# Performance work log

Hardware: AMD Instinct MI355X
Metric: run time of the kernel (lower is better)

## Reference

```python
import jax, jax.numpy as jnp
import numpy as np

NUM_EMBEDDINGS = 8192
EMBEDDING_DIM = 128
COMMITMENT_COST = 0.02


def _l2_normalize(x, axis=-1, eps=1e-12):
    # matches torch F.normalize: x / max(||x||, eps)
    n = jnp.sqrt(jnp.sum(x * x, axis=axis, keepdims=True))
    return x / jnp.maximum(n, eps)


def setup_inputs() -> dict:
    key = jax.random.key(0)
    k1, k2 = jax.random.split(key)
    inputs = jax.random.normal(k1, (16, 128, 2048), dtype=jnp.float32)  # [B, D, T]
    lim = 1.0 / NUM_EMBEDDINGS
    codebook = jax.random.uniform(k2, (NUM_EMBEDDINGS, EMBEDDING_DIM),
                                  dtype=jnp.float32, minval=-lim, maxval=lim)
    return {"inputs": inputs, "codebook": codebook}


def reference(inputs, codebook):
    # inputs: [B, D, T] -> [B, T, D]
    x = jnp.transpose(inputs, (0, 2, 1))
    B, T, D = x.shape
    flat = x.reshape(-1, D)                      # [N, D]
    flat_n = _l2_normalize(flat, axis=1)         # [N, D]
    emb_n = _l2_normalize(codebook, axis=1)      # [K, D]
    # cosine-style distance: 2 - 2 * <x_hat, e_hat>
    distances = 2.0 - 2.0 * jnp.einsum('nd,kd->nk', flat_n, emb_n)  # [N, K]
    encoding_indices = jnp.argmin(distances, axis=1)[:, None]       # [N, 1]
    # (dead-code revival is a training-time RNG side effect on the codebook;
    #  eval path / reference math skips it)
    quantized = codebook[encoding_indices[:, 0]].reshape(B, T, D)   # [B, T, D]
    sg = jax.lax.stop_gradient
    e_latent_loss = jnp.mean((sg(quantized) - x) ** 2)
    q_latent_loss = jnp.mean((quantized - sg(x)) ** 2)
    loss = q_latent_loss + COMMITMENT_COST * e_latent_loss
    # straight-through estimator
    quantized_st = x + sg(quantized - x)
    out = jnp.transpose(quantized_st, (0, 2, 1))  # back to [B, D, T]
    return loss, out, encoding_indices
```

## Files before the change

### kernel.cpp

```cpp
#include <hip/hip_runtime.h>
#include <hip/hip_bf16.h>

#define NROWS 32768
#define KCODES 8192
#define DDIM 128
#define TT 2048
#define ETOT 4194304

typedef __attribute__((ext_vector_type(8))) _Float16 f16x8;
typedef __attribute__((ext_vector_type(4))) float f32x4;

__device__ __forceinline__ float pk(float v, int p) {
    return __int_as_float((__float_as_int(v) & 0xFFFFE000) | p);
}

__device__ __forceinline__ void async16(char* lds_uniform, const char* g_perlane) {
    __builtin_amdgcn_global_load_lds(
        (const __attribute__((address_space(1))) unsigned int*)g_perlane,
        (__attribute__((address_space(3))) unsigned int*)lds_uniform,
        16, 0, 0);
}

#define SYNC2 asm volatile("s_waitcnt vmcnt(2) lgkmcnt(0)\n\ts_barrier" ::: "memory")
#define SYNC0 asm volatile("s_waitcnt vmcnt(0) lgkmcnt(0)\n\ts_barrier" ::: "memory")

__global__ void k_en_prep(const float* __restrict__ cb,
                          _Float16* __restrict__ eh) {
    int w = (blockIdx.x * blockDim.x + threadIdx.x) >> 6;
    int l = threadIdx.x & 63;
    if (w >= KCODES) return;
    const float* row = cb + (long)w * DDIM;
    float v0 = row[l], v1 = row[l + 64];
    float ss = v0 * v0 + v1 * v1;
#pragma unroll
    for (int s = 1; s < 64; s <<= 1) ss += __shfl_xor(ss, s, 64);
    float inv = 1.0f / fmaxf(sqrtf(ss), 1e-12f);
    int tile = w >> 4, c = w & 15;
#pragma unroll
    for (int e = 0; e < 2; e++) {
        int d = l + e * 64;
        float v = (e ? v1 : v0) * inv;
        int ks = d >> 5, kq = (d >> 3) & 3, dr = d & 7;
        long off = (long)tile * 2048 + ks * 512 + (kq * 16 + c) * 8 + dr;
        eh[off] = (_Float16)v;
    }
}

__global__ void k_x_prep(const float* __restrict__ in,
                         _Float16* __restrict__ xh) {
    __shared__ float tb[64][65];
    int bid = blockIdx.x;
    int tt0 = (bid & 31) * 64;
    int dd0 = ((bid >> 5) & 1) * 64;
    int b = bid >> 6;
    const float* base = in + (long)b * DDIM * TT;
    int tl = threadIdx.x & 63;
    int dg = threadIdx.x >> 6;
#pragma unroll
    for (int i = 0; i < 16; i++) {
        int dd = dg + i * 4;
        tb[dd][tl] = base[(long)(dd0 + dd) * TT + tt0 + tl];
    }
    __syncthreads();
    int dl = threadIdx.x & 63;
    int tg = threadIdx.x >> 6;
#pragma unroll
    for (int i = 0; i < 16; i++) {
        int t = tg + i * 4;
        long n = (long)b * TT + tt0 + t;
        xh[n * DDIM + dd0 + dl] = (_Float16)tb[dl][t];
    }
}

__device__ __forceinline__ void mfma4(const char* buf, int l,
                                      const f16x8 (&bx)[4][4], f32x4 (&acc)[4]) {
    const f32x4 Z = {0.f, 0.f, 0.f, 0.f};
    f16x8 ah[4];
#pragma unroll
    for (int ks = 0; ks < 4; ks++)
        ah[ks] = *(const f16x8*)(buf + ks * 1024 + l * 16);
    __builtin_amdgcn_s_setprio(1);
#pragma unroll
    for (int nf = 0; nf < 4; nf++) {
        f32x4 a = __builtin_amdgcn_mfma_f32_16x16x32_f16(ah[0], bx[nf][0], Z, 0, 0, 0);
        a = __builtin_amdgcn_mfma_f32_16x16x32_f16(ah[1], bx[nf][1], a, 0, 0, 0);
        a = __builtin_amdgcn_mfma_f32_16x16x32_f16(ah[2], bx[nf][2], a, 0, 0, 0);
        acc[nf] = __builtin_amdgcn_mfma_f32_16x16x32_f16(ah[3], bx[nf][3], a, 0, 0, 0);
    }
    __builtin_amdgcn_s_setprio(0);
}

__device__ __forceinline__ void sel4(const f32x4 (&acc)[4], int PP,
                                     float (&t1)[4], float (&t2)[4], float (&u1)[4]) {
#pragma unroll
    for (int nf = 0; nf < 4; nf++) {
        f32x4 a = acc[nf];
        float s0 = pk(a[0], PP),     s1 = pk(a[1], PP - 1);
        float s2 = pk(a[2], PP - 2), s3 = pk(a[3], PP - 3);
        float h01 = fmaxf(s0, s1), l01 = fminf(s0, s1);
        float h23 = fmaxf(s2, s3), l23 = fminf(s2, s3);
        float m1 = fmaxf(h01, h23);
        float m2 = fmaxf(fminf(h01, h23), fmaxf(l01, l23));
        float n1 = fminf(t1[nf], m1); t1[nf] = fmaxf(t1[nf], m1);
        t2[nf] = fmaxf(t2[nf], n1);
        u1[nf] = fmaxf(u1[nf], m2);
    }
}

__global__ __launch_bounds__(256, 3) void k_main(const _Float16* __restrict__ xh,
                                                 const _Float16* __restrict__ eh,
                                                 int* __restrict__ cand) {
    extern __shared__ char lds[];
    const int tid = threadIdx.x;
    const int l = tid & 63;
    const int w = tid >> 6;
    const int e8 = blockIdx.x & 7;
    const int rb = blockIdx.x >> 3;
    const int col = l & 15, kq = l >> 4;
    const long rbase = (long)rb * 256;

    f16x8 bx[4][4];
#pragma unroll
    for (int nf = 0; nf < 4; nf++) {
        long n = rbase + w * 64 + nf * 16 + col;
#pragma unroll
        for (int ks = 0; ks < 4; ks++)
            bx[nf][ks] = *(const f16x8*)(xh + n * DDIM + ks * 32 + kq * 8);
    }

    const float NEG = __int_as_float(0xFF800000);
    float t1[4], t2[4], u1[4];
#pragma unroll
    for (int i = 0; i < 4; i++) { t1[i] = t2[i] = u1[i] = NEG; }

    int P = 8191 - (e8 * 1024 + kq * 4);

    const char* gsrc = (const char*)eh + (long)e8 * 262144 + w * 1024 + l * 16;
    char* b0 = lds;
    char* b1 = lds + 8192;
    char* b2 = lds + 16384;

    async16(b0 + w * 1024, gsrc);
    async16(b0 + 4096 + w * 1024, gsrc + 4096);
    async16(b1 + w * 1024, gsrc + 8192);
    async16(b1 + 4096 + w * 1024, gsrc + 12288);

    f32x4 accA[4], accB[4];
    int PA, PB;

    SYNC2;
    async16(b2 + w * 1024, gsrc + 2 * 8192);
    async16(b2 + 4096 + w * 1024, gsrc + 2 * 8192 + 4096);
    mfma4(b0, l, bx, accA); PA = P; P -= 16;
    mfma4(b0 + 4096, l, bx, accB); PB = P; P -= 16;
    sel4(accA, PA, t1, t2, u1);
    { char* tp = b0; b0 = b1; b1 = b2; b2 = tp; }

    for (int p = 1; p <= 30; ++p) {
        SYNC2;
        if (p < 30) {
            async16(b2 + w * 1024, gsrc + (long)(p + 2) * 8192);
            async16(b2 + 4096 + w * 1024, gsrc + (long)(p + 2) * 8192 + 4096);
        }
        mfma4(b0, l, bx, accA); PA = P; P -= 16;
        sel4(accB, PB, t1, t2, u1);
        mfma4(b0 + 4096, l, bx, accB); PB = P; P -= 16;
        sel4(accA, PA, t1, t2, u1);
        { char* tp = b0; b0 = b1; b1 = b2; b2 = tp; }
    }
    SYNC0;
    mfma4(b0, l, bx, accA); PA = P; P -= 16;
    sel4(accB, PB, t1, t2, u1);
    mfma4(b0 + 4096, l, bx, accB); PB = P;
    sel4(accA, PA, t1, t2, u1);
    sel4(accB, PB, t1, t2, u1);

    __syncthreads();
    float* mrg = (float*)lds;
#pragma unroll
    for (int nf = 0; nf < 4; nf++) {
        int row = w * 64 + nf * 16 + col;
        int e = kq * 3;
        mrg[row * 13 + e + 0] = t1[nf];
        mrg[row * 13 + e + 1] = t2[nf];
        mrg[row * 13 + e + 2] = u1[nf];
    }
    __syncthreads();
    {
        float s1 = NEG, s2 = NEG;
#pragma unroll 4
        for (int e = 0; e < 12; e++) {
            float v = mrg[tid * 13 + e];
            float a1 = fminf(s1, v); s1 = fmaxf(s1, v);
            s2 = fmaxf(s2, a1);
        }
        long n = rbase + tid;
        int* cp = cand + n * 16 + e8 * 2;
        cp[0] = 8191 - (__float_as_int(s1) & 0x1FFF);
        cp[1] = 8191 - (__float_as_int(s2) & 0x1FFF);
    }
}

__global__ void k_rf(const float* __restrict__ in, const float* __restrict__ cb,
                     const int* __restrict__ cand, float* __restrict__ out,
                     float* __restrict__ idx_f, double* __restrict__ part) {
    __shared__ float xs[16][132];
    __shared__ int sbi[16];
    __shared__ double sd[256];
    const int tid = threadIdx.x;
    const int n0 = blockIdx.x * 16;
    const int b = n0 >> 11, t0 = n0 & 2047;

    {
        int d = tid >> 1, h = tid & 1;
        const float* src = in + ((long)b * DDIM + d) * TT + t0 + h * 8;
        float4 v0 = *(const float4*)src;
        float4 v1 = *(const float4*)(src + 4);
#pragma unroll
        for (int j = 0; j < 4; j++) {
            xs[h * 8 + j][d] = ((const float*)&v0)[j];
            xs[h * 8 + 4 + j][d] = ((const float*)&v1)[j];
        }
    }
    __syncthreads();

    {
        int r = tid >> 4, k = tid & 15;
        int n = n0 + r;
        int c = cand[n * 16 + k];
        const float4* e = (const float4*)(cb + (long)c * DDIM);
        double dot = 0.0, nrm = 0.0;
        for (int d4 = 0; d4 < 32; d4++) {
            float4 q = e[d4];
#pragma unroll
            for (int j = 0; j < 4; j++) {
                double xd = (double)xs[r][d4 * 4 + j];
                double f = (double)((const float*)&q)[j];
                dot += xd * f;
                nrm += f * f;
            }
        }
        double sv = dot / fmax(sqrt(nrm), 1e-12);
#pragma unroll
        for (int s = 1; s < 16; s <<= 1) {
            double osv = __shfl_xor(sv, s, 64);
            int oc = __shfl_xor(c, s, 64);
            if (osv > sv || (osv == sv && oc < c)) { sv = osv; c = oc; }
        }
        if (k == 0) {
            sbi[r] = c;
            idx_f[n] = (float)c;
        }
    }
    __syncthreads();

    {
        int d = tid >> 1, h = tid & 1;
        float* ob = out + ((long)b * DDIM + d) * TT + t0 + h * 8;
        double acc = 0.0;
        float ov[8];
#pragma unroll
        for (int j = 0; j < 8; j++) {
            int rr = h * 8 + j;
            float xv = xs[rr][d];
            float qv = cb[(long)sbi[rr] * DDIM + d];
            float diff = qv - xv;
            ov[j] = xv + diff;
            acc += (double)diff * (double)diff;
        }
        *(float4*)ob = make_float4(ov[0], ov[1], ov[2], ov[3]);
        *(float4*)(ob + 4) = make_float4(ov[4], ov[5], ov[6], ov[7]);
        sd[tid] = acc;
    }
    __syncthreads();
    for (int s = 128; s > 0; s >>= 1) {
        if (tid < s) sd[tid] += sd[tid + s];
        __syncthreads();
    }
    if (tid == 0) part[blockIdx.x] = sd[0];
}

__global__ void k_loss_final(const double* __restrict__ part, int np,
                             float* __restrict__ loss) {
    __shared__ double sd[256];
    double a = 0.0;
    for (int i = threadIdx.x; i < np; i += 256) a += part[i];
    sd[threadIdx.x] = a;
    __syncthreads();
    for (int s = 128; s > 0; s >>= 1) {
        if (threadIdx.x < s) sd[threadIdx.x] += sd[threadIdx.x + s];
        __syncthreads();
    }
    if (threadIdx.x == 0) {
        float m = (float)(sd[0] / (double)ETOT);
        loss[0] = m + 0.02f * m;
    }
}

extern "C" void kernel_launch(void* const* d_in, const int* in_sizes, int n_in,
                              void* d_out, int out_size, void* d_ws, size_t ws_size,
                              hipStream_t stream) {
    const float* inputs = (const float*)d_in[0];
    const float* cb     = (const float*)d_in[1];
    float* outf = (float*)d_out;

    char* ws = (char*)d_ws;
    _Float16* xh = (_Float16*)ws; ws += (long)NROWS * DDIM * 2;
    _Float16* eh = (_Float16*)ws; ws += (long)KCODES * DDIM * 2;
    int* cand    = (int*)ws;      ws += (long)NROWS * 16 * 4;
    double* part = (double*)ws;   ws += 2048 * 8;

    k_en_prep<<<dim3(2048), dim3(256), 0, stream>>>(cb, eh);
    k_x_prep<<<dim3(1024), dim3(256), 0, stream>>>(inputs, xh);
    k_main<<<dim3(1024), dim3(256), 24576, stream>>>(xh, eh, cand);
    k_rf<<<dim3(2048), dim3(256), 0, stream>>>(inputs, cb, cand, outf + 1,
                                               outf + 1 + (long)ETOT, part);
    k_loss_final<<<dim3(1), dim3(256), 0, stream>>>(part, 2048, outf);
}
```

Measured before the change: 138.2 us.

## Merge prep kernels, interleave MFMA chains, unroll triple-buffer rotation with constant offsets

Merges the codebook-normalise and input-transpose prep kernels into one launch, with block index selecting the role. This removes a kernel launch and lets both prep jobs run concurrently. Reorders the MFMA sequence so the four independent accumulator chains are interleaved per k-step, which removes back-to-back dependent MFMAs. Unrolls the triple-buffered LDS pipeline by three so buffer addresses are compile-time offsets instead of rotating pointers, at the cost of more code size.

After: 285.6 us. 107% more time.

```diff
diff --git a/kernel.cpp b/kernel.cpp
--- a/kernel.cpp
+++ b/kernel.cpp
@@ -24,56 +24,56 @@
 #define SYNC2 asm volatile("s_waitcnt vmcnt(2) lgkmcnt(0)\n\ts_barrier" ::: "memory")
 #define SYNC0 asm volatile("s_waitcnt vmcnt(0) lgkmcnt(0)\n\ts_barrier" ::: "memory")
 
-__global__ void k_en_prep(const float* __restrict__ cb,
-                          _Float16* __restrict__ eh) {
-    int w = (blockIdx.x * blockDim.x + threadIdx.x) >> 6;
-    int l = threadIdx.x & 63;
-    if (w >= KCODES) return;
-    const float* row = cb + (long)w * DDIM;
-    float v0 = row[l], v1 = row[l + 64];
-    float ss = v0 * v0 + v1 * v1;
-#pragma unroll
-    for (int s = 1; s < 64; s <<= 1) ss += __shfl_xor(ss, s, 64);
-    float inv = 1.0f / fmaxf(sqrtf(ss), 1e-12f);
-    int tile = w >> 4, c = w & 15;
-#pragma unroll
-    for (int e = 0; e < 2; e++) {
-        int d = l + e * 64;
-        float v = (e ? v1 : v0) * inv;
-        int ks = d >> 5, kq = (d >> 3) & 3, dr = d & 7;
-        long off = (long)tile * 2048 + ks * 512 + (kq * 16 + c) * 8 + dr;
-        eh[off] = (_Float16)v;
-    }
-}
-
-__global__ void k_x_prep(const float* __restrict__ in,
-                         _Float16* __restrict__ xh) {
+__global__ void k_prep(const float* __restrict__ cb, _Float16* __restrict__ eh,
+                       const float* __restrict__ in, _Float16* __restrict__ xh) {
     __shared__ float tb[64][65];
     int bid = blockIdx.x;
-    int tt0 = (bid & 31) * 64;
-    int dd0 = ((bid >> 5) & 1) * 64;
-    int b = bid >> 6;
-    const float* base = in + (long)b * DDIM * TT;
-    int tl = threadIdx.x & 63;
-    int dg = threadIdx.x >> 6;
-#pragma unroll
-    for (int i = 0; i < 16; i++) {
-        int dd = dg + i * 4;
-        tb[dd][tl] = base[(long)(dd0 + dd) * TT + tt0 + tl];
-    }
-    __syncthreads();
-    int dl = threadIdx.x & 63;
-    int tg = threadIdx.x >> 6;
-#pragma unroll
-    for (int i = 0; i < 16; i++) {
-        int t = tg + i * 4;
-        long n = (long)b * TT + tt0 + t;
-        xh[n * DDIM + dd0 + dl] = (_Float16)tb[dl][t];
-    }
-}
-
-__device__ __forceinline__ void mfma4(const char* buf, int l,
-                                      const f16x8 (&bx)[4][4], f32x4 (&acc)[4]) {
+    if (bid < 2048) {
+        int w = (bid * blockDim.x + threadIdx.x) >> 6;
+        int l = threadIdx.x & 63;
+        if (w >= KCODES) return;
+        const float* row = cb + (long)w * DDIM;
+        float v0 = row[l], v1 = row[l + 64];
+        float ss = v0 * v0 + v1 * v1;
+#pragma unroll
+        for (int s = 1; s < 64; s <<= 1) ss += __shfl_xor(ss, s, 64);
+        float inv = 1.0f / fmaxf(sqrtf(ss), 1e-12f);
+        int tile = w >> 4, c = w & 15;
+#pragma unroll
+        for (int e = 0; e < 2; e++) {
+            int d = l + e * 64;
+            float v = (e ? v1 : v0) * inv;
+            int ks = d >> 5, kq = (d >> 3) & 3, dr = d & 7;
+            long off = (long)tile * 2048 + ks * 512 + (kq * 16 + c) * 8 + dr;
+            eh[off] = (_Float16)v;
+        }
+    } else {
+        bid -= 2048;
+        int tt0 = (bid & 31) * 64;
+        int dd0 = ((bid >> 5) & 1) * 64;
+        int b = bid >> 6;
+        const float* base = in + (long)b * DDIM * TT;
+        int tl = threadIdx.x & 63;
+        int dg = threadIdx.x >> 6;
+#pragma unroll
+        for (int i = 0; i < 16; i++) {
+            int dd = dg + i * 4;
+            tb[dd][tl] = base[(long)(dd0 + dd) * TT + tt0 + tl];
+        }
+        __syncthreads();
+        int dl = threadIdx.x & 63;
+        int tg = threadIdx.x >> 6;
+#pragma unroll
+        for (int i = 0; i < 16; i++) {
+            int t = tg + i * 4;
+            long n = (long)b * TT + tt0 + t;
+            xh[n * DDIM + dd0 + dl] = (_Float16)tb[dl][t];
+        }
+    }
+}
+
+__device__ __forceinline__ void mfma4i(const char* buf, int l,
+                                       const f16x8 (&bx)[4][4], f32x4 (&acc)[4]) {
     const f32x4 Z = {0.f, 0.f, 0.f, 0.f};
     f16x8 ah[4];
 #pragma unroll
@@ -81,12 +81,13 @@
         ah[ks] = *(const f16x8*)(buf + ks * 1024 + l * 16);
     __builtin_amdgcn_s_setprio(1);
 #pragma unroll
-    for (int nf = 0; nf < 4; nf++) {
-        f32x4 a = __builtin_amdgcn_mfma_f32_16x16x32_f16(ah[0], bx[nf][0], Z, 0, 0, 0);
-        a = __builtin_amdgcn_mfma_f32_16x16x32_f16(ah[1], bx[nf][1], a, 0, 0, 0);
-        a = __builtin_amdgcn_mfma_f32_16x16x32_f16(ah[2], bx[nf][2], a, 0, 0, 0);
-        acc[nf] = __builtin_amdgcn_mfma_f32_16x16x32_f16(ah[3], bx[nf][3], a, 0, 0, 0);
-    }
+    for (int nf = 0; nf < 4; nf++)
+        acc[nf] = __builtin_amdgcn_mfma_f32_16x16x32_f16(ah[0], bx[nf][0], Z, 0, 0, 0);
+#pragma unroll
+    for (int ks = 1; ks < 4; ks++)
+#pragma unroll
+        for (int nf = 0; nf < 4; nf++)
+            acc[nf] = __builtin_amdgcn_mfma_f32_16x16x32_f16(ah[ks], bx[nf][ks], acc[nf], 0, 0, 0);
     __builtin_amdgcn_s_setprio(0);
 }
 
@@ -136,42 +137,49 @@
     int P = 8191 - (e8 * 1024 + kq * 4);
 
     const char* gsrc = (const char*)eh + (long)e8 * 262144 + w * 1024 + l * 16;
-    char* b0 = lds;
-    char* b1 = lds + 8192;
-    char* b2 = lds + 16384;
-
-    async16(b0 + w * 1024, gsrc);
-    async16(b0 + 4096 + w * 1024, gsrc + 4096);
-    async16(b1 + w * 1024, gsrc + 8192);
-    async16(b1 + 4096 + w * 1024, gsrc + 12288);
+    const int wo = w * 1024;
+
+    async16(lds + wo, gsrc);
+    async16(lds + 4096 + wo, gsrc + 4096);
+    async16(lds + 8192 + wo, gsrc + 8192);
+    async16(lds + 8192 + 4096 + wo, gsrc + 12288);
 
     f32x4 accA[4], accB[4];
     int PA, PB;
 
     SYNC2;
-    async16(b2 + w * 1024, gsrc + 2 * 8192);
-    async16(b2 + 4096 + w * 1024, gsrc + 2 * 8192 + 4096);
-    mfma4(b0, l, bx, accA); PA = P; P -= 16;
-    mfma4(b0 + 4096, l, bx, accB); PB = P; P -= 16;
+    async16(lds + 16384 + wo, gsrc + 2 * 8192);
+    async16(lds + 16384 + 4096 + wo, gsrc + 2 * 8192 + 4096);
+    mfma4i(lds, l, bx, accA); PA = P; P -= 16;
+    mfma4i(lds + 4096, l, bx, accB); PB = P; P -= 16;
     sel4(accA, PA, t1, t2, u1);
-    { char* tp = b0; b0 = b1; b1 = b2; b2 = tp; }
-
-    for (int p = 1; p <= 30; ++p) {
-        SYNC2;
-        if (p < 30) {
-            async16(b2 + w * 1024, gsrc + (long)(p + 2) * 8192);
-            async16(b2 + 4096 + w * 1024, gsrc + (long)(p + 2) * 8192 + 4096);
-        }
-        mfma4(b0, l, bx, accA); PA = P; P -= 16;
-        sel4(accB, PB, t1, t2, u1);
-        mfma4(b0 + 4096, l, bx, accB); PB = P; P -= 16;
-        sel4(accA, PA, t1, t2, u1);
-        { char* tp = b0; b0 = b1; b1 = b2; b2 = tp; }
-    }
+
+#define PHASE(RD, ST, PHN)                                                     \
+    {                                                                          \
+        SYNC2;                                                                 \
+        if ((PHN) < 30) {                                                      \
+            async16(lds + (ST) + wo, gsrc + (long)((PHN) + 2) * 8192);         \
+            async16(lds + (ST) + 4096 + wo,                                    \
+                    gsrc + (long)((PHN) + 2) * 8192 + 4096);                   \
+        }                                                                      \
+        mfma4i(lds + (RD), l, bx, accA); PA = P; P -= 16;                      \
+        sel4(accB, PB, t1, t2, u1);                                            \
+        mfma4i(lds + (RD) + 4096, l, bx, accB); PB = P; P -= 16;               \
+        sel4(accA, PA, t1, t2, u1);                                            \
+    }
+
+    for (int i = 0; i < 10; ++i) {
+        int p = 3 * i;
+        PHASE(8192,  0,     p + 1);
+        PHASE(16384, 8192,  p + 2);
+        PHASE(0,     16384, p + 3);
+    }
+#undef PHASE
+
     SYNC0;
-    mfma4(b0, l, bx, accA); PA = P; P -= 16;
+    mfma4i(lds + 8192, l, bx, accA); PA = P; P -= 16;
     sel4(accB, PB, t1, t2, u1);
-    mfma4(b0 + 4096, l, bx, accB); PB = P;
+    mfma4i(lds + 8192 + 4096, l, bx, accB); PB = P;
     sel4(accA, PA, t1, t2, u1);
     sel4(accB, PB, t1, t2, u1);
 
@@ -310,8 +318,7 @@
     int* cand    = (int*)ws;      ws += (long)NROWS * 16 * 4;
     double* part = (double*)ws;   ws += 2048 * 8;
 
-    k_en_prep<<<dim3(2048), dim3(256), 0, stream>>>(cb, eh);
-    k_x_prep<<<dim3(1024), dim3(256), 0, stream>>>(inputs, xh);
+    k_prep<<<dim3(3072), dim3(256), 0, stream>>>(cb, eh, inputs, xh);
     k_main<<<dim3(1024), dim3(256), 24576, stream>>>(xh, eh, cand);
     k_rf<<<dim3(2048), dim3(256), 0, stream>>>(inputs, cb, cand, outf + 1,
                                                outf + 1 + (long)ETOT, part);
```
